# Optimization experiments

Measured on AMD Instinct MI355X. Metric: run time of the kernel, lower is better.

Reference implementation:

```python
import jax, jax.numpy as jnp
import numpy as np


def _mlp2(x, w1, b1, w2, b2):
    # 2-layer MLP with exact GELU (matches torch nn.GELU default)
    h = jax.nn.gelu(x @ w1 + b1, approximate=False)
    return h @ w2 + b2


def setup_inputs() -> dict:
    B, nx = 16, 16384
    d_latent, d_hidden, k = 64, 128, 3
    key = jax.random.key(0)
    ks = jax.random.split(key, 14)
    s = 0.1
    inp = {
        "u0": jax.random.normal(ks[0], (B, nx), dtype=jnp.float32),
        "x": jax.random.uniform(ks[1], (B, nx), dtype=jnp.float32),
        # node_mlp: 2 -> d_hidden -> d_latent
        "node_w1": jax.random.normal(ks[2], (2, d_hidden), dtype=jnp.float32) * s,
        "node_b1": jnp.zeros((d_hidden,), dtype=jnp.float32),
        "node_w2": jax.random.normal(ks[3], (d_hidden, d_latent), dtype=jnp.float32) * s,
        "node_b2": jnp.zeros((d_latent,), dtype=jnp.float32),
        # edge_mlp: 3 -> d_hidden -> d_latent
        "edge_w1": jax.random.normal(ks[4], (3, d_hidden), dtype=jnp.float32) * s,
        "edge_b1": jnp.zeros((d_hidden,), dtype=jnp.float32),
        "edge_w2": jax.random.normal(ks[5], (d_hidden, d_latent), dtype=jnp.float32) * s,
        "edge_b2": jnp.zeros((d_latent,), dtype=jnp.float32),
        # combine: 2*d_latent -> d_hidden -> d_latent
        "comb_w1": jax.random.normal(ks[6], (2 * d_latent, d_hidden), dtype=jnp.float32) * s,
        "comb_b1": jnp.zeros((d_hidden,), dtype=jnp.float32),
        "comb_w2": jax.random.normal(ks[7], (d_hidden, d_latent), dtype=jnp.float32) * s,
        "comb_b2": jnp.zeros((d_latent,), dtype=jnp.float32),
        "k": k,
    }
    return inp


def reference(u0, x, node_w1, node_b1, node_w2, node_b2,
              edge_w1, edge_b1, edge_w2, edge_b2,
              comb_w1, comb_b1, comb_w2, comb_b2, k):
    B, nx = u0.shape
    # h_self = node_mlp([u_i, x_i])                       -> [B, nx, d_latent]
    h_self = _mlp2(jnp.stack([u0, x], axis=-1), node_w1, node_b1, node_w2, node_b2)

    # Replicate-padded neighbor gather == clamp indices to [0, nx-1]
    offs = jnp.arange(-k, k + 1)                          # [2k+1]
    idx = jnp.clip(jnp.arange(nx)[None, :] + offs[:, None], 0, nx - 1)  # [2k+1, nx]
    u_j = u0[:, idx]                                      # [B, 2k+1, nx]
    dx = x[:, idx] - x[:, None, :]                        # [B, 2k+1, nx]
    u_i = jnp.broadcast_to(u0[:, None, :], u_j.shape)

    # edge_mlp over all neighbors at once, then sum over neighbor axis
    edge_in = jnp.stack([u_i, u_j, dx], axis=-1)          # [B, 2k+1, nx, 3]
    agg = _mlp2(edge_in, edge_w1, edge_b1, edge_w2, edge_b2).sum(axis=1)  # [B, nx, d_latent]

    return _mlp2(jnp.concatenate([h_self, agg], axis=-1), comb_w1, comb_b1, comb_w2, comb_b2)
```

## Files before the change

### kernel.cpp

```cpp
#include <hip/hip_runtime.h>
#include <hip/hip_bf16.h>

#define NXc 16384
#define DHc 128
#define DLc 64
#define Kc  3
#define Wc  7
#define Pc  32
#define NTc 256
#define HALO 38
#define RB  272

typedef __attribute__((ext_vector_type(8))) short short8;
typedef __attribute__((ext_vector_type(4))) float f32x4;

#define OFF_U  0
#define OFF_X  160
#define OFF_C  320
#define OFF_HC OFF_C
#define OFF_GN 19776
#define OFF_H2 OFF_GN
#define OFF_S  28480
#define SMEM_BYTES 37184

#define WS_NW2 0
#define WS_EW2 8192
#define WS_CW1 16384
#define WS_CW2 32768
#define WS_TOTAL 40960

#if __has_builtin(__builtin_amdgcn_exp2f)
#define EXP2F(x) __builtin_amdgcn_exp2f(x)
#else
#define EXP2F(x) exp2f(x)
#endif
#if __has_builtin(__builtin_amdgcn_rcpf)
#define RCPF(x) __builtin_amdgcn_rcpf(x)
#else
#define RCPF(x) (1.0f / (x))
#endif

__device__ __forceinline__ float gelu_f(float v) {
    float v2 = v * v;
    float z  = v * fmaf(-0.10294325f, v2, -2.30220838f);
    float e  = EXP2F(z);
    return v * RCPF(1.0f + e);
}

__device__ __forceinline__ unsigned pack_bf16(float a, float b) {
    __hip_bfloat162 t;
    t.x = __float2bfloat16(a);
    t.y = __float2bfloat16(b);
    unsigned r;
    __builtin_memcpy(&r, &t, 4);
    return r;
}

__device__ __forceinline__ void store_bf16x4(void* p, float a, float b, float c, float d) {
    uint2 u;
    u.x = pack_bf16(a, b);
    u.y = pack_bf16(c, d);
    *(uint2*)p = u;
}

__global__ void pack_weights(const float* __restrict__ nw2, const float* __restrict__ ew2,
                             const float* __restrict__ cw1, const float* __restrict__ cw2,
                             __hip_bfloat16* __restrict__ ws)
{
    int idx = blockIdx.x * 256 + threadIdx.x;
    const float* src;
    int N, base, e;
    if (idx < 8192)       { src = nw2; N = 64;  base = WS_NW2; e = idx; }
    else if (idx < 16384) { src = ew2; N = 64;  base = WS_EW2; e = idx - 8192; }
    else if (idx < 32768) { src = cw1; N = 128; base = WS_CW1; e = idx - 16384; }
    else                  { src = cw2; N = 64;  base = WS_CW2; e = idx - 32768; }
    int f = e >> 9, l = (e >> 3) & 63, j = e & 7;
    int nt = f >> 2, kt = f & 3;
    int k = kt * 32 + (l >> 4) * 8 + j;
    int n = nt * 16 + (l & 15);
    ws[base + e] = __float2bfloat16(src[k * N + n]);
}

__global__ __launch_bounds__(NTc, 4)
void lifting_mfma(const float* __restrict__ u0, const float* __restrict__ x,
                  const float* __restrict__ nw1, const float* __restrict__ nb1,
                  const float* __restrict__ nb2, const float* __restrict__ eb1,
                  const float* __restrict__ eb2, const float* __restrict__ cb1,
                  const float* __restrict__ cb2, const float* __restrict__ ew1,
                  const short8* __restrict__ wsv, float* __restrict__ out)
{
    __shared__ char sm[SMEM_BYTES];
    float* s_u = (float*)(sm + OFF_U);
    float* s_x = (float*)(sm + OFF_X);
    float* s_c = (float*)(sm + OFF_C);

    const int tid   = threadIdx.x;
    const int wave  = tid >> 6;
    const int lane  = tid & 63;
    const int quad  = lane >> 4;
    const int l15   = lane & 15;
    const int tiles = NXc / Pc;
    const int b     = blockIdx.x / tiles;
    const int i0    = (blockIdx.x % tiles) * Pc;
    const float* ub = u0 + (size_t)b * NXc;
    const float* xb = x  + (size_t)b * NXc;

    if (tid < HALO) {
        int i = i0 - Kc + tid;
        i = i < 0 ? 0 : (i >= NXc ? NXc - 1 : i);
        s_u[tid] = ub[i];
        s_x[tid] = xb[i];
    }
    __syncthreads();

    for (int idx = tid; idx < HALO * DHc; idx += NTc) {
        int t = idx >> 7, j = idx & 127;
        s_c[idx] = fmaf(s_u[t], ew1[DHc + j], s_x[t] * ew1[2 * DHc + j]);
    }
    for (int idx = tid; idx < Pc * 64; idx += NTc) {
        int p = idx >> 6, jp = (idx & 63) * 2;
        float uu = s_u[p + Kc], xx = s_x[p + Kc];
        float p0 = fmaf(uu, nw1[jp],     fmaf(xx, nw1[DHc + jp],     nb1[jp]));
        float p1 = fmaf(uu, nw1[jp + 1], fmaf(xx, nw1[DHc + jp + 1], nb1[jp + 1]));
        *(unsigned*)(sm + OFF_GN + p * RB + jp * 2) = pack_bf16(gelu_f(p0), gelu_f(p1));
    }
    __syncthreads();

    for (int idx = tid; idx < Pc * 64; idx += NTc) {
        int p = idx >> 6, jp = (idx & 63) * 2;
        float uu = s_u[p + Kc], xx = s_x[p + Kc];
        float a0 = fmaf(uu, ew1[jp],     -(xx * ew1[2 * DHc + jp]))     + eb1[jp];
        float a1 = fmaf(uu, ew1[jp + 1], -(xx * ew1[2 * DHc + jp + 1])) + eb1[jp + 1];
        float acc0 = 0.f, acc1 = 0.f;
        const float* crow = s_c + p * DHc + jp;
        #pragma unroll
        for (int o = 0; o < Wc; ++o) {
            acc0 += gelu_f(a0 + crow[o * DHc]);
            acc1 += gelu_f(a1 + crow[o * DHc + 1]);
        }
        *(unsigned*)(sm + OFF_S + p * RB + jp * 2) = pack_bf16(acc0, acc1);
    }
    __syncthreads();

    {
        const int mt = wave & 1, mat = wave >> 1;
        const int rowbase = mt * 16;
        const int aoff = mat ? OFF_S : OFF_GN;
        const short8* Bmat = wsv + (mat ? (WS_EW2 >> 3) : (WS_NW2 >> 3));
        f32x4 acc[4] = {{0,0,0,0},{0,0,0,0},{0,0,0,0},{0,0,0,0}};
        #pragma unroll
        for (int kt = 0; kt < 4; ++kt) {
            short8 af = *(const short8*)(sm + aoff + (rowbase + l15) * RB + kt * 64 + quad * 16);
            #pragma unroll
            for (int nt = 0; nt < 4; ++nt) {
                short8 wf = Bmat[(nt * 4 + kt) * 64 + lane];
                acc[nt] = __builtin_amdgcn_mfma_f32_16x16x32_bf16(wf, af, acc[nt], 0, 0, 0);
            }
        }
        const float* bias = mat ? eb2 : nb2;
        const float bscale = mat ? 7.f : 1.f;
        const int colhalf = mat ? DLc : 0;
        const int p = rowbase + l15;
        #pragma unroll
        for (int nt = 0; nt < 4; ++nt) {
            float4 bv = ((const float4*)bias)[nt * 4 + quad];
            store_bf16x4(sm + OFF_HC + p * RB + (colhalf + nt * 16 + quad * 4) * 2,
                         fmaf(bscale, bv.x, acc[nt][0]),
                         fmaf(bscale, bv.y, acc[nt][1]),
                         fmaf(bscale, bv.z, acc[nt][2]),
                         fmaf(bscale, bv.w, acc[nt][3]));
        }
    }
    __syncthreads();

    {
        const int mt = wave & 1, nh = wave >> 1;
        const int rowbase = mt * 16;
        const short8* Bmat = wsv + (WS_CW1 >> 3);
        f32x4 acc[4] = {{0,0,0,0},{0,0,0,0},{0,0,0,0},{0,0,0,0}};
        #pragma unroll
        for (int kt = 0; kt < 4; ++kt) {
            short8 af = *(const short8*)(sm + OFF_HC + (rowbase + l15) * RB + kt * 64 + quad * 16);
            #pragma unroll
            for (int t = 0; t < 4; ++t) {
                int nt = nh * 4 + t;
                short8 wf = Bmat[(nt * 4 + kt) * 64 + lane];
                acc[t] = __builtin_amdgcn_mfma_f32_16x16x32_bf16(wf, af, acc[t], 0, 0, 0);
            }
        }
        const int p = rowbase + l15;
        #pragma unroll
        for (int t = 0; t < 4; ++t) {
            int nbase = (nh * 4 + t) * 16 + quad * 4;
            float4 cb = ((const float4*)cb1)[nbase >> 2];
            store_bf16x4(sm + OFF_H2 + p * RB + nbase * 2,
                         gelu_f(acc[t][0] + cb.x),
                         gelu_f(acc[t][1] + cb.y),
                         gelu_f(acc[t][2] + cb.z),
                         gelu_f(acc[t][3] + cb.w));
        }
    }
    __syncthreads();

    {
        const int mt = wave & 1, nh = wave >> 1;
        const int rowbase = mt * 16;
        const short8* Bmat = wsv + (WS_CW2 >> 3);
        f32x4 acc[2] = {{0,0,0,0},{0,0,0,0}};
        #pragma unroll
        for (int kt = 0; kt < 4; ++kt) {
            short8 af = *(const short8*)(sm + OFF_H2 + (rowbase + l15) * RB + kt * 64 + quad * 16);
            #pragma unroll
            for (int t = 0; t < 2; ++t) {
                int nt = nh * 2 + t;
                short8 wf = Bmat[(nt * 4 + kt) * 64 + lane];
                acc[t] = __builtin_amdgcn_mfma_f32_16x16x32_bf16(wf, af, acc[t], 0, 0, 0);
            }
        }
        const int p = rowbase + l15;
        float* outb = out + ((size_t)b * NXc + i0 + p) * DLc;
        #pragma unroll
        for (int t = 0; t < 2; ++t) {
            int nbase = (nh * 2 + t) * 16 + quad * 4;
            float4 cb = ((const float4*)cb2)[nbase >> 2];
            float4 v;
            v.x = acc[t][0] + cb.x;
            v.y = acc[t][1] + cb.y;
            v.z = acc[t][2] + cb.z;
            v.w = acc[t][3] + cb.w;
            *(float4*)(outb + nbase) = v;
        }
    }
}

extern "C" void kernel_launch(void* const* d_in, const int* in_sizes, int n_in,
                              void* d_out, int out_size, void* d_ws, size_t ws_size,
                              hipStream_t stream) {
    const float* u0  = (const float*)d_in[0];
    const float* x   = (const float*)d_in[1];
    const float* nw1 = (const float*)d_in[2];
    const float* nb1 = (const float*)d_in[3];
    const float* nw2 = (const float*)d_in[4];
    const float* nb2 = (const float*)d_in[5];
    const float* ew1 = (const float*)d_in[6];
    const float* eb1 = (const float*)d_in[7];
    const float* ew2 = (const float*)d_in[8];
    const float* eb2 = (const float*)d_in[9];
    const float* cw1 = (const float*)d_in[10];
    const float* cb1 = (const float*)d_in[11];
    const float* cw2 = (const float*)d_in[12];
    const float* cb2 = (const float*)d_in[13];
    float* out = (float*)d_out;

    __hip_bfloat16* ws = (__hip_bfloat16*)d_ws;
    pack_weights<<<WS_TOTAL / 256, 256, 0, stream>>>(nw2, ew2, cw1, cw2, ws);

    const int grid = 16 * (NXc / Pc);
    lifting_mfma<<<grid, NTc, 0, stream>>>(u0, x, nw1, nb1, nb2, eb1, eb2, cb1, cb2,
                                           ew1, (const short8*)d_ws, out);
}
```

Measured before the change: 233.8 us.

## Store edge neighbor partials as bf16 in LDS, fuse node/edge prologue loops

Stores the per-halo edge first-layer partial products as bf16 in a padded LDS layout instead of fp32. This shrinks shared memory per block, and the launch bound is raised to 5 blocks per SM to match. The node GELU and edge neighbor-sum loops are merged into one pass with 4 features per thread, float4 weight loads and an FMA-fused GELU accumulate. The bf16 pack now uses manual round-to-nearest-even bit arithmetic. Rounding the partial sums to bf16 before GELU adds some precision loss, and the higher occupancy target may constrain registers.

```diff
diff --git a/kernel.cpp b/kernel.cpp
--- a/kernel.cpp
+++ b/kernel.cpp
@@ -10,6 +10,7 @@
 #define NTc 256
 #define HALO 38
 #define RB  272
+#define RBc 272
 
 typedef __attribute__((ext_vector_type(8))) short short8;
 typedef __attribute__((ext_vector_type(4))) float f32x4;
@@ -18,10 +19,10 @@
 #define OFF_X  160
 #define OFF_C  320
 #define OFF_HC OFF_C
-#define OFF_GN 19776
+#define OFF_GN 10656
 #define OFF_H2 OFF_GN
-#define OFF_S  28480
-#define SMEM_BYTES 37184
+#define OFF_S  19360
+#define SMEM_BYTES 28064
 
 #define WS_NW2 0
 #define WS_EW2 8192
@@ -40,27 +41,47 @@
 #define RCPF(x) (1.0f / (x))
 #endif
 
+#define GC0 -2.30220838f
+#define GC1 -0.10294325f
+
 __device__ __forceinline__ float gelu_f(float v) {
     float v2 = v * v;
-    float z  = v * fmaf(-0.10294325f, v2, -2.30220838f);
+    float z  = v * fmaf(GC1, v2, GC0);
     float e  = EXP2F(z);
     return v * RCPF(1.0f + e);
 }
 
+__device__ __forceinline__ float gelu_acc(float v, float acc) {
+    float v2 = v * v;
+    float z  = v * fmaf(GC1, v2, GC0);
+    float e  = EXP2F(z);
+    float r  = RCPF(1.0f + e);
+    return fmaf(v, r, acc);
+}
+
+__device__ __forceinline__ unsigned bf16rne(float a) {
+    unsigned u;
+    __builtin_memcpy(&u, &a, 4);
+    return u + 0x7FFFu + ((u >> 16) & 1u);
+}
 __device__ __forceinline__ unsigned pack_bf16(float a, float b) {
-    __hip_bfloat162 t;
-    t.x = __float2bfloat16(a);
-    t.y = __float2bfloat16(b);
-    unsigned r;
-    __builtin_memcpy(&r, &t, 4);
-    return r;
-}
-
+    return (bf16rne(a) >> 16) | (bf16rne(b) & 0xFFFF0000u);
+}
 __device__ __forceinline__ void store_bf16x4(void* p, float a, float b, float c, float d) {
     uint2 u;
     u.x = pack_bf16(a, b);
     u.y = pack_bf16(c, d);
     *(uint2*)p = u;
+}
+__device__ __forceinline__ float bf_lo(unsigned u) {
+    unsigned v = u << 16;
+    float f; __builtin_memcpy(&f, &v, 4);
+    return f;
+}
+__device__ __forceinline__ float bf_hi(unsigned u) {
+    unsigned v = u & 0xFFFF0000u;
+    float f; __builtin_memcpy(&f, &v, 4);
+    return f;
 }
 
 __global__ void pack_weights(const float* __restrict__ nw2, const float* __restrict__ ew2,
@@ -81,7 +102,7 @@
     ws[base + e] = __float2bfloat16(src[k * N + n]);
 }
 
-__global__ __launch_bounds__(NTc, 4)
+__global__ __launch_bounds__(NTc, 5)
 void lifting_mfma(const float* __restrict__ u0, const float* __restrict__ x,
                   const float* __restrict__ nw1, const float* __restrict__ nb1,
                   const float* __restrict__ nb2, const float* __restrict__ eb1,
@@ -92,7 +113,6 @@
     __shared__ char sm[SMEM_BYTES];
     float* s_u = (float*)(sm + OFF_U);
     float* s_x = (float*)(sm + OFF_X);
-    float* s_c = (float*)(sm + OFF_C);
 
     const int tid   = threadIdx.x;
     const int wave  = tid >> 6;
@@ -113,32 +133,48 @@
     }
     __syncthreads();
 
-    for (int idx = tid; idx < HALO * DHc; idx += NTc) {
-        int t = idx >> 7, j = idx & 127;
-        s_c[idx] = fmaf(s_u[t], ew1[DHc + j], s_x[t] * ew1[2 * DHc + j]);
-    }
-    for (int idx = tid; idx < Pc * 64; idx += NTc) {
-        int p = idx >> 6, jp = (idx & 63) * 2;
+    for (int idx = tid; idx < HALO * 64; idx += NTc) {
+        int t = idx >> 6, j2 = idx & 63;
+        int j = j2 * 2;
+        float uu = s_u[t], xx = s_x[t];
+        float c0 = fmaf(uu, ew1[DHc + j],     xx * ew1[2 * DHc + j]);
+        float c1 = fmaf(uu, ew1[DHc + j + 1], xx * ew1[2 * DHc + j + 1]);
+        *(unsigned*)(sm + OFF_C + t * RBc + j2 * 4) = pack_bf16(c0, c1);
+    }
+    __syncthreads();
+
+    for (int idx = tid; idx < Pc * 32; idx += NTc) {
+        int p = idx >> 5, jq = idx & 31;
+        int j0 = jq * 4;
         float uu = s_u[p + Kc], xx = s_x[p + Kc];
-        float p0 = fmaf(uu, nw1[jp],     fmaf(xx, nw1[DHc + jp],     nb1[jp]));
-        float p1 = fmaf(uu, nw1[jp + 1], fmaf(xx, nw1[DHc + jp + 1], nb1[jp + 1]));
-        *(unsigned*)(sm + OFF_GN + p * RB + jp * 2) = pack_bf16(gelu_f(p0), gelu_f(p1));
-    }
-    __syncthreads();
-
-    for (int idx = tid; idx < Pc * 64; idx += NTc) {
-        int p = idx >> 6, jp = (idx & 63) * 2;
-        float uu = s_u[p + Kc], xx = s_x[p + Kc];
-        float a0 = fmaf(uu, ew1[jp],     -(xx * ew1[2 * DHc + jp]))     + eb1[jp];
-        float a1 = fmaf(uu, ew1[jp + 1], -(xx * ew1[2 * DHc + jp + 1])) + eb1[jp + 1];
-        float acc0 = 0.f, acc1 = 0.f;
-        const float* crow = s_c + p * DHc + jp;
+
+        float4 w0 = *(const float4*)(nw1 + j0);
+        float4 w1 = *(const float4*)(nw1 + DHc + j0);
+        float4 nb = *(const float4*)(nb1 + j0);
+        float g0 = gelu_f(fmaf(uu, w0.x, fmaf(xx, w1.x, nb.x)));
+        float g1 = gelu_f(fmaf(uu, w0.y, fmaf(xx, w1.y, nb.y)));
+        float g2 = gelu_f(fmaf(uu, w0.z, fmaf(xx, w1.z, nb.z)));
+        float g3 = gelu_f(fmaf(uu, w0.w, fmaf(xx, w1.w, nb.w)));
+        store_bf16x4(sm + OFF_GN + p * RB + j0 * 2, g0, g1, g2, g3);
+
+        float4 e0 = *(const float4*)(ew1 + j0);
+        float4 e2 = *(const float4*)(ew1 + 2 * DHc + j0);
+        float4 be = *(const float4*)(eb1 + j0);
+        float a0 = fmaf(uu, e0.x, -(xx * e2.x)) + be.x;
+        float a1 = fmaf(uu, e0.y, -(xx * e2.y)) + be.y;
+        float a2 = fmaf(uu, e0.z, -(xx * e2.z)) + be.z;
+        float a3 = fmaf(uu, e0.w, -(xx * e2.w)) + be.w;
+        float acc0 = 0.f, acc1 = 0.f, acc2 = 0.f, acc3 = 0.f;
+        const char* crow = sm + OFF_C + p * RBc + jq * 8;
         #pragma unroll
         for (int o = 0; o < Wc; ++o) {
-            acc0 += gelu_f(a0 + crow[o * DHc]);
-            acc1 += gelu_f(a1 + crow[o * DHc + 1]);
-        }
-        *(unsigned*)(sm + OFF_S + p * RB + jp * 2) = pack_bf16(acc0, acc1);
+            uint2 cp = *(const uint2*)(crow + o * RBc);
+            acc0 = gelu_acc(a0 + bf_lo(cp.x), acc0);
+            acc1 = gelu_acc(a1 + bf_hi(cp.x), acc1);
+            acc2 = gelu_acc(a2 + bf_lo(cp.y), acc2);
+            acc3 = gelu_acc(a3 + bf_hi(cp.y), acc3);
+        }
+        store_bf16x4(sm + OFF_S + p * RB + j0 * 2, acc0, acc1, acc2, acc3);
     }
     __syncthreads();
 
```

Result: faster. 205.8 us (-12.0%).
